# Optimization experiments

Measured on AMD Instinct MI355X. Metric: run time of the kernel, lower is better.

Reference implementation:

```python
import jax, jax.numpy as jnp
import numpy as np

B, L, H = 32, 2048, 512


def setup_inputs() -> dict:
    key = jax.random.key(0)
    k1, k2, k3, k4, k5, k6 = jax.random.split(key, 6)
    scale = 1.0 / np.sqrt(H)
    return {
        "query": jax.random.normal(k1, (B, H), dtype=jnp.float32),
        "ref": jax.random.normal(k2, (B, L, H), dtype=jnp.float32),
        "mask": jax.random.randint(k3, (B, L), 0, 2) == 1,
        # learned params (torch Linear weight layout: [out, in]; apply as x @ W.T)
        "W_ref": jax.random.normal(k4, (H, H), dtype=jnp.float32) * scale,
        "W_q": jax.random.normal(k5, (H, H), dtype=jnp.float32) * scale,
        "v": jax.random.normal(k6, (H,), dtype=jnp.float32) * scale,
    }


def reference(query, ref, mask, W_ref, W_q, v):
    scale = 1.0 / np.sqrt(H)
    # additive (Bahdanau) scores: v^T tanh(W_ref ref + W_q q)
    encoded_ref = jnp.einsum("blh,oh->blo", ref, W_ref)          # (B, L, H)
    encoded_q = jnp.einsum("bh,oh->bo", query, W_q)[:, None, :]  # (B, 1, H)
    scores = jnp.einsum("blh,h->bl", jnp.tanh(encoded_ref + encoded_q), v)
    scores = scores * scale
    scores = jnp.where(mask, -1e9, scores)
    attn = jax.nn.softmax(scores, axis=1)                         # (B, L)
    glimpse = jnp.einsum("bl,blh->bh", attn, ref)                 # (B, H)
    return glimpse, scores
```

## Files before the change

### kernel.cpp

```cpp
#include <hip/hip_runtime.h>
#include <hip/hip_bf16.h>
#include <cstdint>

typedef __attribute__((ext_vector_type(4))) float f32x4;
typedef __attribute__((ext_vector_type(8))) short s16x8;

#define NB   32
#define NL   2048
#define NH   512
#define NM   (NB * NL)
#define SCALE 0.04419417382415922f
#define LDST 36

__device__ __forceinline__ ushort f2bf(float f) {
    __hip_bfloat16 b = __float2bfloat16(f);
    return *reinterpret_cast<ushort*>(&b);
}

__global__ __launch_bounds__(256) void k_convW(const float* __restrict__ W,
                                               ushort* __restrict__ Wb) {
    int i = blockIdx.x * 256 + threadIdx.x;
    const float4* s = (const float4*)W;
    float4 a = s[2 * i], c = s[2 * i + 1];
    union { ushort u[8]; int4 v; } p;
    p.u[0] = f2bf(a.x); p.u[1] = f2bf(a.y); p.u[2] = f2bf(a.z); p.u[3] = f2bf(a.w);
    p.u[4] = f2bf(c.x); p.u[5] = f2bf(c.y); p.u[6] = f2bf(c.z); p.u[7] = f2bf(c.w);
    ((int4*)Wb)[i] = p.v;
}

__global__ __launch_bounds__(512) void k_eq(const float* __restrict__ query,
                                            const float* __restrict__ Wq,
                                            float* __restrict__ eq) {
    int b = blockIdx.x;
    int o = threadIdx.x;
    __shared__ float q[NH];
    q[o] = query[b * NH + o];
    __syncthreads();
    const float4* w = (const float4*)(Wq + (size_t)o * NH);
    float acc = 0.f;
#pragma unroll 4
    for (int i = 0; i < NH / 4; ++i) {
        float4 x = w[i];
        acc += q[4 * i] * x.x + q[4 * i + 1] * x.y + q[4 * i + 2] * x.z + q[4 * i + 3] * x.w;
    }
    eq[b * NH + o] = acc;
}

__global__ __launch_bounds__(256) void k_gemm(const float* __restrict__ ref,
                                              const ushort* __restrict__ Wb,
                                              const float* __restrict__ eq,
                                              const float* __restrict__ v,
                                              float* __restrict__ part) {
    __shared__ ushort As[128 * LDST];
    __shared__ ushort Bs[128 * LDST];

    int tid = threadIdx.x;
    int lane = tid & 63, wid = tid >> 6;
    int wr = wid >> 1, wc = wid & 1;

    int phys = blockIdx.x;
    int xcd = phys & 7, slot = phys >> 3;
    int mt = xcd * 64 + (slot >> 2);
    int nt = slot & 3;
    int m0 = mt * 128, n0 = nt * 128;
    int b = mt >> 4;

    f32x4 acc[4][4];
#pragma unroll
    for (int i = 0; i < 4; ++i)
#pragma unroll
        for (int j = 0; j < 4; ++j) acc[i][j] = (f32x4)(0.f);

    int srow = tid >> 1, sks = (tid & 1) * 16;
    const float*  asrc = ref + (size_t)(m0 + srow) * NH + sks;
    const ushort* bsrc = Wb + (size_t)(n0 + srow) * NH + sks;
    int awr = srow * LDST + sks;

    int lr = lane & 15, kq = lane >> 4;
    int aoff[4], boff[4];
#pragma unroll
    for (int f = 0; f < 4; ++f) {
        aoff[f] = (wr * 64 + f * 16 + lr) * LDST + kq * 8;
        boff[f] = (wc * 64 + f * 16 + lr) * LDST + kq * 8;
    }

    float4 pa0, pa1, pa2, pa3;
    int4 pb0, pb1;
    {
        const float* s = asrc;
        pa0 = *(const float4*)(s);
        pa1 = *(const float4*)(s + 4);
        pa2 = *(const float4*)(s + 8);
        pa3 = *(const float4*)(s + 12);
        const int4* bs = (const int4*)(bsrc);
        pb0 = bs[0];
        pb1 = bs[1];
    }

    for (int kt = 0; kt < 16; ++kt) {
        union { ushort u[8]; int4 v; } p0, p1;
        p0.u[0] = f2bf(pa0.x); p0.u[1] = f2bf(pa0.y); p0.u[2] = f2bf(pa0.z); p0.u[3] = f2bf(pa0.w);
        p0.u[4] = f2bf(pa1.x); p0.u[5] = f2bf(pa1.y); p0.u[6] = f2bf(pa1.z); p0.u[7] = f2bf(pa1.w);
        p1.u[0] = f2bf(pa2.x); p1.u[1] = f2bf(pa2.y); p1.u[2] = f2bf(pa2.z); p1.u[3] = f2bf(pa2.w);
        p1.u[4] = f2bf(pa3.x); p1.u[5] = f2bf(pa3.y); p1.u[6] = f2bf(pa3.z); p1.u[7] = f2bf(pa3.w);
        *(int4*)&As[awr] = p0.v;
        *(int4*)&As[awr + 8] = p1.v;
        *(int4*)&Bs[awr] = pb0;
        *(int4*)&Bs[awr + 8] = pb1;
        __syncthreads();

        if (kt < 15) {
            const float* s = asrc + (kt + 1) * 32;
            pa0 = *(const float4*)(s);
            pa1 = *(const float4*)(s + 4);
            pa2 = *(const float4*)(s + 8);
            pa3 = *(const float4*)(s + 12);
            const int4* bs = (const int4*)(bsrc + (kt + 1) * 32);
            pb0 = bs[0];
            pb1 = bs[1];
        }

        s16x8 af[4], bf[4];
#pragma unroll
        for (int f = 0; f < 4; ++f) af[f] = *(const s16x8*)&As[aoff[f]];
#pragma unroll
        for (int f = 0; f < 4; ++f) bf[f] = *(const s16x8*)&Bs[boff[f]];
        __syncthreads();

#pragma unroll
        for (int fr = 0; fr < 4; ++fr)
#pragma unroll
            for (int fc = 0; fc < 4; ++fc)
                acc[fr][fc] = __builtin_amdgcn_mfma_f32_16x16x32_bf16(
                    af[fr], bf[fc], acc[fr][fc], 0, 0, 0);
    }

    const float* eqb = eq + b * NH;
    float vv[4], ee[4];
#pragma unroll
    for (int fc = 0; fc < 4; ++fc) {
        int c = n0 + wc * 64 + fc * 16 + lr;
        vv[fc] = v[c];
        ee[fc] = eqb[c];
    }
#pragma unroll
    for (int fr = 0; fr < 4; ++fr) {
#pragma unroll
        for (int reg = 0; reg < 4; ++reg) {
            float s = 0.f;
#pragma unroll
            for (int fc = 0; fc < 4; ++fc) {
                float x = acc[fr][fc][reg] + ee[fc];
                float t = 1.f - 2.f / (__expf(2.f * x) + 1.f);
                s += vv[fc] * t;
            }
            s += __shfl_xor(s, 1);
            s += __shfl_xor(s, 2);
            s += __shfl_xor(s, 4);
            s += __shfl_xor(s, 8);
            if (lr == 0) {
                int row = wr * 64 + fr * 16 + kq * 4 + reg;
                part[(size_t)nt * NM + m0 + row] = s;
            }
        }
    }
}

__global__ __launch_bounds__(256) void k_softmax(const float* __restrict__ part,
                                                 const int* __restrict__ mask,
                                                 float* __restrict__ out_sc,
                                                 float* __restrict__ attn) {
    int b = blockIdx.x;
    int tid = threadIdx.x;
    int lane = tid & 63, wid = tid >> 6;
    __shared__ float red[4];
    float sc[8];
    float mx = -3.4e38f;
#pragma unroll
    for (int i = 0; i < 8; ++i) {
        int m = b * NL + i * 256 + tid;
        float s = (part[m] + part[NM + m] + part[2 * NM + m] + part[3 * NM + m]) * SCALE;
        if (mask[m] != 0) s = -1e9f;
        out_sc[m] = s;
        sc[i] = s;
        mx = fmaxf(mx, s);
    }
#pragma unroll
    for (int o = 32; o >= 1; o >>= 1) mx = fmaxf(mx, __shfl_xor(mx, o));
    if (lane == 0) red[wid] = mx;
    __syncthreads();
    mx = fmaxf(fmaxf(red[0], red[1]), fmaxf(red[2], red[3]));
    __syncthreads();
    float ls = 0.f;
#pragma unroll
    for (int i = 0; i < 8; ++i) {
        float e = __expf(sc[i] - mx);
        sc[i] = e;
        ls += e;
    }
#pragma unroll
    for (int o = 32; o >= 1; o >>= 1) ls += __shfl_xor(ls, o);
    if (lane == 0) red[wid] = ls;
    __syncthreads();
    float inv = 1.f / (red[0] + red[1] + red[2] + red[3]);
#pragma unroll
    for (int i = 0; i < 8; ++i) attn[b * NL + i * 256 + tid] = sc[i] * inv;
}

__global__ __launch_bounds__(256) void k_glp(const float* __restrict__ ref,
                                             const float* __restrict__ attn,
                                             float* __restrict__ glp) {
    int sp = blockIdx.x, b = blockIdx.y;
    int tid = threadIdx.x;
    const float* attb = attn + b * NL + sp * 128;
    float2 acc = make_float2(0.f, 0.f);
#pragma unroll 4
    for (int l = 0; l < 128; ++l) {
        float a = attb[l];
        const float2* row = (const float2*)(ref + (size_t)(b * NL + sp * 128 + l) * NH);
        float2 r = row[tid];
        acc.x += a * r.x;
        acc.y += a * r.y;
    }
    ((float2*)(glp + (size_t)(sp * NB + b) * NH))[tid] = acc;
}

__global__ __launch_bounds__(256) void k_gred(const float* __restrict__ glp,
                                              float* __restrict__ out_gl) {
    int idx = blockIdx.x * 256 + threadIdx.x;
    float s = 0.f;
#pragma unroll
    for (int sp = 0; sp < 16; ++sp) s += glp[sp * (NB * NH) + idx];
    out_gl[idx] = s;
}

extern "C" void kernel_launch(void* const* d_in, const int* in_sizes, int n_in,
                              void* d_out, int out_size, void* d_ws, size_t ws_size,
                              hipStream_t stream) {
    const float* query = (const float*)d_in[0];
    const float* ref   = (const float*)d_in[1];
    const int*   mask  = (const int*)d_in[2];
    const float* W_ref = (const float*)d_in[3];
    const float* W_q   = (const float*)d_in[4];
    const float* v     = (const float*)d_in[5];

    float* out_gl = (float*)d_out;
    float* out_sc = out_gl + NB * NH;

    char* w = (char*)d_ws;
    ushort* wW  = (ushort*)w;
    float* eq   = (float*)(w + 524288);
    float* part = (float*)(w + 589824);
    float* attn = (float*)(w + 1638400);
    float* glp  = (float*)(w + 1900544);

    k_convW<<<128, 256, 0, stream>>>(W_ref, wW);
    k_eq<<<NB, 512, 0, stream>>>(query, W_q, eq);
    k_gemm<<<2048, 256, 0, stream>>>(ref, wW, eq, v, part);
    k_softmax<<<NB, 256, 0, stream>>>(part, mask, out_sc, attn);
    k_glp<<<dim3(16, NB), 256, 0, stream>>>(ref, attn, glp);
    k_gred<<<64, 256, 0, stream>>>(glp, out_gl);
}
```

Baseline: 128.6 us.

## Double-buffer LDS tiles in GEMM with one barrier per k-step

Switches the GEMM's shared-memory A/B tiles to two buffers. Each k-iteration reads fragments from the current buffer, writes the next tile (already converted to bf16) into the other buffer, and prefetches global data two steps ahead, all before the MFMAs. This drops one of the two __syncthreads per iteration and overlaps LDS stores with compute, at the cost of doubling LDS use (about 36KB per block), which may lower occupancy.

```diff
diff --git a/kernel.cpp b/kernel.cpp
--- a/kernel.cpp
+++ b/kernel.cpp
@@ -11,6 +11,7 @@
 #define NM   (NB * NL)
 #define SCALE 0.04419417382415922f
 #define LDST 36
+#define BUFO (128 * LDST)
 
 __device__ __forceinline__ ushort f2bf(float f) {
     __hip_bfloat16 b = __float2bfloat16(f);
@@ -51,8 +52,8 @@
                                               const float* __restrict__ eq,
                                               const float* __restrict__ v,
                                               float* __restrict__ part) {
-    __shared__ ushort As[128 * LDST];
-    __shared__ ushort Bs[128 * LDST];
+    __shared__ ushort As[2 * BUFO];
+    __shared__ ushort Bs[2 * BUFO];
 
     int tid = threadIdx.x;
     int lane = tid & 63, wid = tid >> 6;
@@ -95,9 +96,6 @@
         const int4* bs = (const int4*)(bsrc);
         pb0 = bs[0];
         pb1 = bs[1];
-    }
-
-    for (int kt = 0; kt < 16; ++kt) {
         union { ushort u[8]; int4 v; } p0, p1;
         p0.u[0] = f2bf(pa0.x); p0.u[1] = f2bf(pa0.y); p0.u[2] = f2bf(pa0.z); p0.u[3] = f2bf(pa0.w);
         p0.u[4] = f2bf(pa1.x); p0.u[5] = f2bf(pa1.y); p0.u[6] = f2bf(pa1.z); p0.u[7] = f2bf(pa1.w);
@@ -107,32 +105,58 @@
         *(int4*)&As[awr + 8] = p1.v;
         *(int4*)&Bs[awr] = pb0;
         *(int4*)&Bs[awr + 8] = pb1;
-        __syncthreads();
+        const float* s1 = asrc + 32;
+        pa0 = *(const float4*)(s1);
+        pa1 = *(const float4*)(s1 + 4);
+        pa2 = *(const float4*)(s1 + 8);
+        pa3 = *(const float4*)(s1 + 12);
+        const int4* bs1 = (const int4*)(bsrc + 32);
+        pb0 = bs1[0];
+        pb1 = bs1[1];
+    }
+    __syncthreads();
+
+    for (int kt = 0; kt < 16; ++kt) {
+        int cur = kt & 1;
+        const ushort* Ac = As + cur * BUFO;
+        const ushort* Bc = Bs + cur * BUFO;
+        ushort* An = (ushort*)As + (cur ^ 1) * BUFO;
+        ushort* Bn = (ushort*)Bs + (cur ^ 1) * BUFO;
+
+        s16x8 af[4], bf[4];
+#pragma unroll
+        for (int f = 0; f < 4; ++f) af[f] = *(const s16x8*)&Ac[aoff[f]];
+#pragma unroll
+        for (int f = 0; f < 4; ++f) bf[f] = *(const s16x8*)&Bc[boff[f]];
 
         if (kt < 15) {
-            const float* s = asrc + (kt + 1) * 32;
+            union { ushort u[8]; int4 v; } p0, p1;
+            p0.u[0] = f2bf(pa0.x); p0.u[1] = f2bf(pa0.y); p0.u[2] = f2bf(pa0.z); p0.u[3] = f2bf(pa0.w);
+            p0.u[4] = f2bf(pa1.x); p0.u[5] = f2bf(pa1.y); p0.u[6] = f2bf(pa1.z); p0.u[7] = f2bf(pa1.w);
+            p1.u[0] = f2bf(pa2.x); p1.u[1] = f2bf(pa2.y); p1.u[2] = f2bf(pa2.z); p1.u[3] = f2bf(pa2.w);
+            p1.u[4] = f2bf(pa3.x); p1.u[5] = f2bf(pa3.y); p1.u[6] = f2bf(pa3.z); p1.u[7] = f2bf(pa3.w);
+            *(int4*)&An[awr] = p0.v;
+            *(int4*)&An[awr + 8] = p1.v;
+            *(int4*)&Bn[awr] = pb0;
+            *(int4*)&Bn[awr + 8] = pb1;
+        }
+        if (kt < 14) {
+            const float* s = asrc + (kt + 2) * 32;
             pa0 = *(const float4*)(s);
             pa1 = *(const float4*)(s + 4);
             pa2 = *(const float4*)(s + 8);
             pa3 = *(const float4*)(s + 12);
-            const int4* bs = (const int4*)(bsrc + (kt + 1) * 32);
+            const int4* bs = (const int4*)(bsrc + (kt + 2) * 32);
             pb0 = bs[0];
             pb1 = bs[1];
         }
-
-        s16x8 af[4], bf[4];
-#pragma unroll
-        for (int f = 0; f < 4; ++f) af[f] = *(const s16x8*)&As[aoff[f]];
-#pragma unroll
-        for (int f = 0; f < 4; ++f) bf[f] = *(const s16x8*)&Bs[boff[f]];
-        __syncthreads();
-
 #pragma unroll
         for (int fr = 0; fr < 4; ++fr)
 #pragma unroll
             for (int fc = 0; fc < 4; ++fc)
                 acc[fr][fc] = __builtin_amdgcn_mfma_f32_16x16x32_bf16(
                     af[fr], bf[fc], acc[fr][fc], 0, 0, 0);
+        __syncthreads();
     }
 
     const float* eqb = eq + b * NH;
```

New measurement: 242.2 us. +88.4%, slower.

## Pre-convert ref to bf16 and stage GEMM tiles via direct global-to-LDS loads

Applied to the files above, without the earlier changes.

Adds a pass that converts the whole ref tensor to bf16 in workspace. The GEMM then streams bf16 tiles straight into double-buffered LDS with global_load_lds, and the glimpse reduction reads the bf16 copy too. The aim is to remove in-loop fp32-to-bf16 conversion and halve the bytes the GEMM and glimpse kernels read. The cost is an extra full read of fp32 ref plus a 64MB write, unpadded LDS rows that may cause bank conflicts, and lower glimpse precision. The new path runs only when the workspace is large enough; otherwise the old fp32 kernels are kept.

```diff
diff --git a/kernel.cpp b/kernel.cpp
--- a/kernel.cpp
+++ b/kernel.cpp
@@ -10,11 +10,20 @@
 #define NH   512
 #define NM   (NB * NL)
 #define SCALE 0.04419417382415922f
-#define LDST 36
 
 __device__ __forceinline__ ushort f2bf(float f) {
     __hip_bfloat16 b = __float2bfloat16(f);
     return *reinterpret_cast<ushort*>(&b);
+}
+__device__ __forceinline__ float bf2f(unsigned u) {
+    union { unsigned u; float f; } a; a.u = u << 16; return a.f;
+}
+
+__device__ __forceinline__ void gl16(const ushort* g, ushort* l) {
+    __builtin_amdgcn_global_load_lds(
+        (const __attribute__((address_space(1))) unsigned int*)g,
+        (__attribute__((address_space(3))) unsigned int*)l,
+        16, 0, 0);
 }
 
 __global__ __launch_bounds__(256) void k_convW(const float* __restrict__ W,
@@ -26,6 +35,23 @@
     p.u[0] = f2bf(a.x); p.u[1] = f2bf(a.y); p.u[2] = f2bf(a.z); p.u[3] = f2bf(a.w);
     p.u[4] = f2bf(c.x); p.u[5] = f2bf(c.y); p.u[6] = f2bf(c.z); p.u[7] = f2bf(c.w);
     ((int4*)Wb)[i] = p.v;
+}
+
+__global__ __launch_bounds__(256) void k_convRef(const float* __restrict__ ref,
+                                                 ushort* __restrict__ refb) {
+    int i = blockIdx.x * 256 + threadIdx.x;
+    const float4* s = (const float4*)ref;
+#pragma unroll
+    for (int it = 0; it < 8; ++it) {
+        int idx = it * 4194304 / 8 * 2;
+        int ci = i + it * 524288;
+        float4 a = s[2 * ci], c = s[2 * ci + 1];
+        union { ushort u[8]; int4 v; } p;
+        p.u[0] = f2bf(a.x); p.u[1] = f2bf(a.y); p.u[2] = f2bf(a.z); p.u[3] = f2bf(a.w);
+        p.u[4] = f2bf(c.x); p.u[5] = f2bf(c.y); p.u[6] = f2bf(c.z); p.u[7] = f2bf(c.w);
+        ((int4*)refb)[ci] = p.v;
+        (void)idx;
+    }
 }
 
 __global__ __launch_bounds__(512) void k_eq(const float* __restrict__ query,
@@ -46,13 +72,13 @@
     eq[b * NH + o] = acc;
 }
 
-__global__ __launch_bounds__(256) void k_gemm(const float* __restrict__ ref,
-                                              const ushort* __restrict__ Wb,
-                                              const float* __restrict__ eq,
-                                              const float* __restrict__ v,
-                                              float* __restrict__ part) {
-    __shared__ ushort As[128 * LDST];
-    __shared__ ushort Bs[128 * LDST];
+__global__ __launch_bounds__(256) void k_gemm_bf(const ushort* __restrict__ refb,
+                                                 const ushort* __restrict__ Wb,
+                                                 const float* __restrict__ eq,
+                                                 const float* __restrict__ v,
+                                                 float* __restrict__ part) {
+    __shared__ ushort As[2][128 * 32];
+    __shared__ ushort Bs[2][128 * 32];
 
     int tid = threadIdx.x;
     int lane = tid & 63, wid = tid >> 6;
@@ -71,69 +97,56 @@
 #pragma unroll
         for (int j = 0; j < 4; ++j) acc[i][j] = (f32x4)(0.f);
 
-    int srow = tid >> 1, sks = (tid & 1) * 16;
-    const float*  asrc = ref + (size_t)(m0 + srow) * NH + sks;
-    const ushort* bsrc = Wb + (size_t)(n0 + srow) * NH + sks;
-    int awr = srow * LDST + sks;
+    int cc = wid * 2;
+    int grow = lane >> 2, gcol = (lane & 3) * 8;
+    const ushort* aglob = refb + (size_t)(m0 + cc * 16 + grow) * NH + gcol;
+    const ushort* bglob = Wb + (size_t)(n0 + cc * 16 + grow) * NH + gcol;
 
     int lr = lane & 15, kq = lane >> 4;
     int aoff[4], boff[4];
 #pragma unroll
     for (int f = 0; f < 4; ++f) {
-        aoff[f] = (wr * 64 + f * 16 + lr) * LDST + kq * 8;
-        boff[f] = (wc * 64 + f * 16 + lr) * LDST + kq * 8;
-    }
-
-    float4 pa0, pa1, pa2, pa3;
-    int4 pb0, pb1;
-    {
-        const float* s = asrc;
-        pa0 = *(const float4*)(s);
-        pa1 = *(const float4*)(s + 4);
-        pa2 = *(const float4*)(s + 8);
-        pa3 = *(const float4*)(s + 12);
-        const int4* bs = (const int4*)(bsrc);
-        pb0 = bs[0];
-        pb1 = bs[1];
-    }
-
-    for (int kt = 0; kt < 16; ++kt) {
-        union { ushort u[8]; int4 v; } p0, p1;
-        p0.u[0] = f2bf(pa0.x); p0.u[1] = f2bf(pa0.y); p0.u[2] = f2bf(pa0.z); p0.u[3] = f2bf(pa0.w);
-        p0.u[4] = f2bf(pa1.x); p0.u[5] = f2bf(pa1.y); p0.u[6] = f2bf(pa1.z); p0.u[7] = f2bf(pa1.w);
-        p1.u[0] = f2bf(pa2.x); p1.u[1] = f2bf(pa2.y); p1.u[2] = f2bf(pa2.z); p1.u[3] = f2bf(pa2.w);
-        p1.u[4] = f2bf(pa3.x); p1.u[5] = f2bf(pa3.y); p1.u[6] = f2bf(pa3.z); p1.u[7] = f2bf(pa3.w);
-        *(int4*)&As[awr] = p0.v;
-        *(int4*)&As[awr + 8] = p1.v;
-        *(int4*)&Bs[awr] = pb0;
-        *(int4*)&Bs[awr + 8] = pb1;
+        aoff[f] = (wr * 64 + f * 16 + lr) * 32 + kq * 8;
+        boff[f] = (wc * 64 + f * 16 + lr) * 32 + kq * 8;
+    }
+
+#define STAGE(buf, kt)                                      \
+    {   gl16(aglob + (kt) * 32, &As[buf][cc * 512]);        \
+        gl16(aglob + (kt) * 32 + 16 * NH, &As[buf][(cc + 1) * 512]); \
+        gl16(bglob + (kt) * 32, &Bs[buf][cc * 512]);        \
+        gl16(bglob + (kt) * 32 + 16 * NH, &Bs[buf][(cc + 1) * 512]); }
+
+#define READ_FRAGS(buf)                                     \
+    _Pragma("unroll")                                       \
+    for (int f = 0; f < 4; ++f) af[f] = *(const s16x8*)&As[buf][aoff[f]]; \
+    _Pragma("unroll")                                       \
+    for (int f = 0; f < 4; ++f) bfr[f] = *(const s16x8*)&Bs[buf][boff[f]];
+
+#define DO_MFMA()                                           \
+    _Pragma("unroll")                                       \
+    for (int fr = 0; fr < 4; ++fr)                          \
+        _Pragma("unroll")                                   \
+        for (int fc = 0; fc < 4; ++fc)                      \
+            acc[fr][fc] = __builtin_amdgcn_mfma_f32_16x16x32_bf16(af[fr], bfr[fc], acc[fr][fc], 0, 0, 0);
+
+    STAGE(0, 0)
+    __syncthreads();
+
+    for (int t2 = 0; t2 < 8; ++t2) {
+        s16x8 af[4], bfr[4];
+        int k0 = 2 * t2;
+        if (k0 + 1 < 16) STAGE(1, k0 + 1)
+        READ_FRAGS(0)
+        DO_MFMA()
         __syncthreads();
-
-        if (kt < 15) {
-            const float* s = asrc + (kt + 1) * 32;
-            pa0 = *(const float4*)(s);
-            pa1 = *(const float4*)(s + 4);
-            pa2 = *(const float4*)(s + 8);
-            pa3 = *(const float4*)(s + 12);
-            const int4* bs = (const int4*)(bsrc + (kt + 1) * 32);
-            pb0 = bs[0];
-            pb1 = bs[1];
-        }
-
-        s16x8 af[4], bf[4];
-#pragma unroll
-        for (int f = 0; f < 4; ++f) af[f] = *(const s16x8*)&As[aoff[f]];
-#pragma unroll
-        for (int f = 0; f < 4; ++f) bf[f] = *(const s16x8*)&Bs[boff[f]];
+        if (k0 + 2 < 16) STAGE(0, k0 + 2)
+        READ_FRAGS(1)
+        DO_MFMA()
         __syncthreads();
-
-#pragma unroll
-        for (int fr = 0; fr < 4; ++fr)
-#pragma unroll
-            for (int fc = 0; fc < 4; ++fc)
-                acc[fr][fc] = __builtin_amdgcn_mfma_f32_16x16x32_bf16(
-                    af[fr], bf[fc], acc[fr][fc], 0, 0, 0);
-    }
+    }
+#undef STAGE
+#undef READ_FRAGS
+#undef DO_MFMA
 
     const float* eqb = eq + b * NH;
     float vv[4], ee[4];
@@ -166,6 +179,104 @@
     }
 }
 
+#define LDST 36
+__global__ __launch_bounds__(256) void k_gemm_f32(const float* __restrict__ ref,
+                                                  const ushort* __restrict__ Wb,
+                                                  const float* __restrict__ eq,
+                                                  const float* __restrict__ v,
+                                                  float* __restrict__ part) {
+    __shared__ ushort As[128 * LDST];
+    __shared__ ushort Bs[128 * LDST];
+    int tid = threadIdx.x;
+    int lane = tid & 63, wid = tid >> 6;
+    int wr = wid >> 1, wc = wid & 1;
+    int phys = blockIdx.x;
+    int xcd = phys & 7, slot = phys >> 3;
+    int mt = xcd * 64 + (slot >> 2);
+    int nt = slot & 3;
+    int m0 = mt * 128, n0 = nt * 128;
+    int b = mt >> 4;
+    f32x4 acc[4][4];
+#pragma unroll
+    for (int i = 0; i < 4; ++i)
+#pragma unroll
+        for (int j = 0; j < 4; ++j) acc[i][j] = (f32x4)(0.f);
+    int srow = tid >> 1, sks = (tid & 1) * 16;
+    const float*  asrc = ref + (size_t)(m0 + srow) * NH + sks;
+    const ushort* bsrc = Wb + (size_t)(n0 + srow) * NH + sks;
+    int awr = srow * LDST + sks;
+    int lr = lane & 15, kq = lane >> 4;
+    int aoff[4], boff[4];
+#pragma unroll
+    for (int f = 0; f < 4; ++f) {
+        aoff[f] = (wr * 64 + f * 16 + lr) * LDST + kq * 8;
+        boff[f] = (wc * 64 + f * 16 + lr) * LDST + kq * 8;
+    }
+    float4 pa0, pa1, pa2, pa3;
+    int4 pb0, pb1;
+    {
+        const float* s = asrc;
+        pa0 = *(const float4*)(s); pa1 = *(const float4*)(s + 4);
+        pa2 = *(const float4*)(s + 8); pa3 = *(const float4*)(s + 12);
+        const int4* bs = (const int4*)(bsrc);
+        pb0 = bs[0]; pb1 = bs[1];
+    }
+    for (int kt = 0; kt < 16; ++kt) {
+        union { ushort u[8]; int4 v; } p0, p1;
+        p0.u[0] = f2bf(pa0.x); p0.u[1] = f2bf(pa0.y); p0.u[2] = f2bf(pa0.z); p0.u[3] = f2bf(pa0.w);
+        p0.u[4] = f2bf(pa1.x); p0.u[5] = f2bf(pa1.y); p0.u[6] = f2bf(pa1.z); p0.u[7] = f2bf(pa1.w);
+        p1.u[0] = f2bf(pa2.x); p1.u[1] = f2bf(pa2.y); p1.u[2] = f2bf(pa2.z); p1.u[3] = f2bf(pa2.w);
+        p1.u[4] = f2bf(pa3.x); p1.u[5] = f2bf(pa3.y); p1.u[6] = f2bf(pa3.z); p1.u[7] = f2bf(pa3.w);
+        *(int4*)&As[awr] = p0.v; *(int4*)&As[awr + 8] = p1.v;
+        *(int4*)&Bs[awr] = pb0;  *(int4*)&Bs[awr + 8] = pb1;
+        __syncthreads();
+        if (kt < 15) {
+            const float* s = asrc + (kt + 1) * 32;
+            pa0 = *(const float4*)(s); pa1 = *(const float4*)(s + 4);
+            pa2 = *(const float4*)(s + 8); pa3 = *(const float4*)(s + 12);
+            const int4* bs = (const int4*)(bsrc + (kt + 1) * 32);
+            pb0 = bs[0]; pb1 = bs[1];
+        }
+        s16x8 af[4], bfr[4];
+#pragma unroll
+        for (int f = 0; f < 4; ++f) af[f] = *(const s16x8*)&As[aoff[f]];
+#pragma unroll
+        for (int f = 0; f < 4; ++f) bfr[f] = *(const s16x8*)&Bs[boff[f]];
+        __syncthreads();
+#pragma unroll
+        for (int fr = 0; fr < 4; ++fr)
+#pragma unroll
+            for (int fc = 0; fc < 4; ++fc)
+                acc[fr][fc] = __builtin_amdgcn_mfma_f32_16x16x32_bf16(af[fr], bfr[fc], acc[fr][fc], 0, 0, 0);
+    }
+    const float* eqb = eq + b * NH;
+    float vv[4], ee[4];
+#pragma unroll
+    for (int fc = 0; fc < 4; ++fc) {
+        int c = n0 + wc * 64 + fc * 16 + lr;
+        vv[fc] = v[c]; ee[fc] = eqb[c];
+    }
+#pragma unroll
+    for (int fr = 0; fr < 4; ++fr) {
+#pragma unroll
+        for (int reg = 0; reg < 4; ++reg) {
+            float s = 0.f;
+#pragma unroll
+            for (int fc = 0; fc < 4; ++fc) {
+                float x = acc[fr][fc][reg] + ee[fc];
+                float t = 1.f - 2.f / (__expf(2.f * x) + 1.f);
+                s += vv[fc] * t;
+            }
+            s += __shfl_xor(s, 1); s += __shfl_xor(s, 2);
+            s += __shfl_xor(s, 4); s += __shfl_xor(s, 8);
+            if (lr == 0) {
+                int row = wr * 64 + fr * 16 + kq * 4 + reg;
+                part[(size_t)nt * NM + m0 + row] = s;
+            }
+        }
+    }
+}
+
 __global__ __launch_bounds__(256) void k_softmax(const float* __restrict__ part,
                                                  const int* __restrict__ mask,
                                                  float* __restrict__ out_sc,
@@ -207,9 +318,26 @@
     for (int i = 0; i < 8; ++i) attn[b * NL + i * 256 + tid] = sc[i] * inv;
 }
 
-__global__ __launch_bounds__(256) void k_glp(const float* __restrict__ ref,
-                                             const float* __restrict__ attn,
-                                             float* __restrict__ glp) {
+__global__ __launch_bounds__(256) void k_glp_bf(const ushort* __restrict__ refb,
+                                                const float* __restrict__ attn,
+                                                float* __restrict__ glp) {
+    int sp = blockIdx.x, b = blockIdx.y;
+    int tid = threadIdx.x;
+    const float* attb = attn + b * NL + sp * 128;
+    float2 acc = make_float2(0.f, 0.f);
+#pragma unroll 4
+    for (int l = 0; l < 128; ++l) {
+        float a = attb[l];
+        unsigned r = ((const unsigned*)(refb + (size_t)(b * NL + sp * 128 + l) * NH))[tid];
+        acc.x += a * bf2f(r & 0xFFFFu);
+        acc.y += a * bf2f(r >> 16);
+    }
+    ((float2*)(glp + (size_t)(sp * NB + b) * NH))[tid] = acc;
+}
+
+__global__ __launch_bounds__(256) void k_glp_f32(const float* __restrict__ ref,
+                                                 const float* __restrict__ attn,
+                                                 float* __restrict__ glp) {
     int sp = blockIdx.x, b = blockIdx.y;
     int tid = threadIdx.x;
     const float* attb = attn + b * NL + sp * 128;
@@ -249,15 +377,32 @@
 
     char* w = (char*)d_ws;
     ushort* wW  = (ushort*)w;
-    float* eq   = (float*)(w + 524288);
-    float* part = (float*)(w + 589824);
-    float* attn = (float*)(w + 1638400);
-    float* glp  = (float*)(w + 1900544);
-
-    k_convW<<<128, 256, 0, stream>>>(W_ref, wW);
-    k_eq<<<NB, 512, 0, stream>>>(query, W_q, eq);
-    k_gemm<<<2048, 256, 0, stream>>>(ref, wW, eq, v, part);
-    k_softmax<<<NB, 256, 0, stream>>>(part, mask, out_sc, attn);
-    k_glp<<<dim3(16, NB), 256, 0, stream>>>(ref, attn, glp);
-    k_gred<<<64, 256, 0, stream>>>(glp, out_gl);
-}
+
+    if (ws_size >= (size_t)70100000) {
+        ushort* refb = (ushort*)(w + 524288);
+        float* eq    = (float*)(w + 524288 + 67108864);
+        float* part  = (float*)(w + 524288 + 67108864 + 65536);
+        float* attn  = (float*)(w + 524288 + 67108864 + 65536 + 1048576);
+        float* glp   = (float*)(w + 524288 + 67108864 + 65536 + 1048576 + 262144);
+
+        k_convW<<<128, 256, 0, stream>>>(W_ref, wW);
+        k_convRef<<<2048, 256, 0, stream>>>(ref, refb);
+        k_eq<<<NB, 512, 0, stream>>>(query, W_q, eq);
+        k_gemm_bf<<<2048, 256, 0, stream>>>(refb, wW, eq, v, part);
+        k_softmax<<<NB, 256, 0, stream>>>(part, mask, out_sc, attn);
+        k_glp_bf<<<dim3(16, NB), 256, 0, stream>>>(refb, attn, glp);
+        k_gred<<<64, 256, 0, stream>>>(glp, out_gl);
+    } else {
+        float* eq   = (float*)(w + 524288);
+        float* part = (float*)(w + 589824);
+        float* attn = (float*)(w + 1638400);
+        float* glp  = (float*)(w + 1900544);
+
+        k_convW<<<128, 256, 0, stream>>>(W_ref, wW);
+        k_eq<<<NB, 512, 0, stream>>>(query, W_q, eq);
+        k_gemm_f32<<<2048, 256, 0, stream>>>(ref, wW, eq, v, part);
+        k_softmax<<<NB, 256, 0, stream>>>(part, mask, out_sc, attn);
+        k_glp_f32<<<dim3(16, NB), 256, 0, stream>>>(ref, attn, glp);
+        k_gred<<<64, 256, 0, stream>>>(glp, out_gl);
+    }
+}
```

After: 145.9 us. +13.5%, slower.
